# Kernel optimization log

Hardware: AMD Instinct MI355X
Metric: run time of the kernel (lower is better)

The kernel has to match this reference:

```python
import jax, jax.numpy as jnp
import numpy as np

B, T, C, H = 2, 2048, 1024, 16
HD = C // H  # head dim = 64


def setup_inputs() -> dict:
    key = jax.random.key(0)
    k0, k1, k2 = jax.random.split(key, 3)
    x = jax.random.normal(k0, (B, T, C), jnp.float32)
    W_attn = jax.random.normal(k1, (C, 3 * C), jnp.float32) * 0.02
    b_attn = jnp.zeros((3 * C,), jnp.float32)
    W_proj = jax.random.normal(k2, (C, C), jnp.float32) * 0.02
    b_proj = jnp.zeros((C,), jnp.float32)
    # rope: (1,1,T,HD//2,2,2) stack of 2x2 rotation matrices [[cos,-sin],[sin,cos]]
    inv_freq = 1.0 / (10000.0 ** (jnp.arange(0, HD, 2, dtype=jnp.float32) / HD))
    ang = jnp.arange(T, dtype=jnp.float32)[:, None] * inv_freq[None, :]  # (T, HD//2)
    cos, sin = jnp.cos(ang), jnp.sin(ang)
    rope = jnp.stack([jnp.stack([cos, -sin], -1), jnp.stack([sin, cos], -1)], -2)
    rope = rope[None, None]  # (1,1,T,HD//2,2,2)
    return dict(x=x, W_attn=W_attn, b_attn=b_attn, W_proj=W_proj, b_proj=b_proj, rope=rope)


def reference(x, W_attn, b_attn, W_proj, b_proj, rope):
    Bv, Tv, Cv = x.shape
    Hd = Cv // H
    qkv = x @ W_attn + b_attn                      # (B,T,3C) fused QKV proj
    q, k, v = jnp.split(qkv, 3, axis=-1)

    def heads(t):
        return t.reshape(Bv, Tv, H, Hd).transpose(0, 2, 1, 3)  # (B,H,T,Hd)

    q, k, v = heads(q), heads(k), heads(v)

    cos = rope[..., 0, 0][..., None]               # (1,1,T,Hd//2,1)
    sin = rope[..., 1, 0][..., None]

    def rot(t):
        tr = t.reshape(Bv, H, Tv, Hd // 2, 2)
        xr, yr = tr[..., 0:1], tr[..., 1:2]
        out = jnp.concatenate([xr * cos - yr * sin, xr * sin + yr * cos], axis=-1)
        return out.reshape(Bv, H, Tv, Hd)

    q, k = rot(q), rot(k)

    scale = 1.0 / np.sqrt(Hd).astype(np.float32)
    att = jnp.einsum('bhqd,bhkd->bhqk', q, k) * scale
    mask = jnp.tril(jnp.ones((Tv, Tv), dtype=bool))  # causal
    att = jnp.where(mask[None, None], att, -jnp.inf)
    att = jax.nn.softmax(att, axis=-1)
    y = jnp.einsum('bhqk,bhkd->bhqd', att, v)
    y = y.transpose(0, 2, 1, 3).reshape(Bv, Tv, Cv)
    return y @ W_proj + b_proj
```

## Files before the change

kernel.cpp:

```cpp
#include <hip/hip_runtime.h>
#include <hip/hip_bf16.h>

typedef __attribute__((ext_vector_type(8))) short short8;
typedef __attribute__((ext_vector_type(4))) short short4b;
typedef __attribute__((ext_vector_type(4))) float f32x4;
typedef __attribute__((ext_vector_type(16))) float f32x16;
typedef __attribute__((ext_vector_type(4))) unsigned u32x4;

static constexpr int Bb = 2, Tt = 2048, Cc = 1024, Hh = 16;
static constexpr int BT = Bb * Tt;
static constexpr int N1 = 3 * Cc;
static constexpr float QS = 0.125f * 1.44269504f;

__device__ __forceinline__ unsigned short f2b(float f) {
  union { float f; unsigned u; } v; v.f = f;
  unsigned r = v.u + 0x7fffu + ((v.u >> 16) & 1u);
  return (unsigned short)(r >> 16);
}
__device__ __forceinline__ float b2f(short s) {
  union { unsigned u; float f; } v; v.u = ((unsigned)(unsigned short)s) << 16;
  return v.f;
}

__global__ __launch_bounds__(256) void k_cast(const float* __restrict__ in,
                                              unsigned short* __restrict__ out, int n) {
  int i = (blockIdx.x * 256 + threadIdx.x) * 8;
  if (i >= n) return;
  float4 a = *reinterpret_cast<const float4*>(in + i);
  float4 b = *reinterpret_cast<const float4*>(in + i + 4);
  short8 o;
  o[0] = f2b(a.x); o[1] = f2b(a.y); o[2] = f2b(a.z); o[3] = f2b(a.w);
  o[4] = f2b(b.x); o[5] = f2b(b.y); o[6] = f2b(b.z); o[7] = f2b(b.w);
  *reinterpret_cast<short8*>(out + i) = o;
}

__global__ __launch_bounds__(256) void k_tcast(const float* __restrict__ in,
                                               unsigned short* __restrict__ out,
                                               int R, int Ccol) {
  __shared__ float tile[32][33];
  int cb = blockIdx.x * 32, rb = blockIdx.y * 32;
  int tx = threadIdx.x & 31, ty = threadIdx.x >> 5;
  for (int i = 0; i < 32; i += 8)
    tile[ty + i][tx] = in[(size_t)(rb + ty + i) * Ccol + cb + tx];
  __syncthreads();
  for (int i = 0; i < 32; i += 8)
    out[(size_t)(cb + ty + i) * R + rb + tx] = f2b(tile[tx][ty + i]);
}

template <int NF, int EPI>
__global__ __launch_bounds__(512, 2)
void k_gemm8(const unsigned short* __restrict__ A, const unsigned short* __restrict__ Bt,
             const float* __restrict__ bias, void* __restrict__ Cout,
             const float* __restrict__ rope, unsigned short* __restrict__ Qs,
             unsigned short* __restrict__ Ks, unsigned short* __restrict__ Vt,
             int M, int N, int K) {
  constexpr int BN = NF * 64;
  constexpr int ASZ = 256 * 64;
  constexpr int BSZ = BN * 64;
  constexpr int STRIDE = ASZ + BSZ;
  extern __shared__ unsigned short lds[];
  const int tid = threadIdx.x, lane = tid & 63, w = tid >> 6;
  const int wm = w >> 2, wn = w & 3;
  const int l15 = lane & 15, l4 = lane >> 4;
  int nbx = gridDim.x;
  int lin = blockIdx.y * nbx + blockIdx.x;
  int cpx = (nbx * gridDim.y) >> 3;
  lin = (lin & 7) * cpx + (lin >> 3);
  const int mb = lin / nbx, nb = lin % nbx;
  const size_t arow0 = (size_t)mb * 256;
  const size_t brow0 = (size_t)nb * BN;

  const int srow = lane >> 3;
  const int scol = (((lane & 7) * 16) ^ (srow << 4)) >> 1;
  auto stage = [&](int buf, int k0) {
    unsigned short* Ab = lds + buf * STRIDE;
    unsigned short* Bb = Ab + ASZ;
#pragma unroll
    for (int i = 0; i < 4; i++) {
      int c = w + 8 * i;
      const unsigned short* g = A + (arow0 + c * 8 + srow) * (size_t)K + k0 + scol;
      __builtin_amdgcn_global_load_lds((const __attribute__((address_space(1))) void*)g,
          (__attribute__((address_space(3))) void*)(Ab + c * 512), 16, 0, 0);
    }
#pragma unroll
    for (int i = 0; i < NF; i++) {
      int c = w + 8 * i;
      const unsigned short* g = Bt + (brow0 + c * 8 + srow) * (size_t)K + k0 + scol;
      __builtin_amdgcn_global_load_lds((const __attribute__((address_space(1))) void*)g,
          (__attribute__((address_space(3))) void*)(Bb + c * 512), 16, 0, 0);
    }
  };

  f32x4 acc[8][NF] = {};
  const int NK = K >> 6;

  stage(0, 0);
  asm volatile("s_waitcnt vmcnt(0)" ::: "memory");
  asm volatile("s_barrier" ::: "memory");

  for (int kt = 0; kt < NK; kt++) {
    int buf = kt & 1;
    if (kt + 1 < NK) stage(buf ^ 1, (kt + 1) << 6);
    const unsigned short* Ab = lds + buf * STRIDE;
    const unsigned short* Bb = Ab + ASZ;
    short8 af[8][2];
#pragma unroll
    for (int p = 0; p < NF; p++) {
      if (p == 0) {
#pragma unroll
        for (int m = 0; m < 8; m++) {
          int ra = wm * 128 + m * 16 + l15;
#pragma unroll
          for (int kk = 0; kk < 2; kk++) {
            int cb = (kk * 64 + l4 * 16) ^ ((ra & 7) << 4);
            af[m][kk] = *reinterpret_cast<const short8*>(Ab + ra * 64 + (cb >> 1));
          }
        }
      }
      short8 bfr[2];
      int rb = wn * (NF * 16) + p * 16 + l15;
#pragma unroll
      for (int kk = 0; kk < 2; kk++) {
        int cb = (kk * 64 + l4 * 16) ^ ((rb & 7) << 4);
        bfr[kk] = *reinterpret_cast<const short8*>(Bb + rb * 64 + (cb >> 1));
      }
      asm volatile("s_barrier" ::: "memory");
      asm volatile("s_waitcnt lgkmcnt(0)" ::: "memory");
      __builtin_amdgcn_sched_barrier(0);
      __builtin_amdgcn_s_setprio(1);
#pragma unroll
      for (int m = 0; m < 8; m++) {
        acc[m][p] = __builtin_amdgcn_mfma_f32_16x16x32_bf16(af[m][0], bfr[0], acc[m][p], 0, 0, 0);
        acc[m][p] = __builtin_amdgcn_mfma_f32_16x16x32_bf16(af[m][1], bfr[1], acc[m][p], 0, 0, 0);
      }
      __builtin_amdgcn_s_setprio(0);
      if (p == NF - 1)
        asm volatile("s_waitcnt vmcnt(0)" ::: "memory");
      asm volatile("s_barrier" ::: "memory");
    }
  }

#pragma unroll
  for (int m = 0; m < 8; m++) {
#pragma unroll
    for (int n = 0; n < NF; n++) {
      int ccol0 = nb * BN + wn * (NF * 16) + n * 16;
      float bv = bias[ccol0 + l15];
      int r0 = mb * 256 + wm * 128 + m * 16 + l4 * 4;
      if (EPI == 0) {
#pragma unroll
        for (int j = 0; j < 4; j++)
          ((float*)Cout)[(size_t)(r0 + j) * N + ccol0 + l15] = acc[m][n][j] + bv;
      } else {
        int cls = ccol0 >> 10;
        int h = (ccol0 >> 6) & 15;
        int d = (ccol0 & 63) + l15;
        int bq = r0 >> 11;
        int t0 = r0 & 2047;
        size_t bh = (size_t)bq * 16 + h;
        if (cls == 2) {
          short4b o;
#pragma unroll
          for (int j = 0; j < 4; j++) o[j] = (short)f2b(acc[m][n][j] + bv);
          *reinterpret_cast<short4b*>(Vt + (bh * 64 + d) * Tt + t0) = o;
        } else {
          unsigned short* dst = (cls == 0) ? Qs : Ks;
          int jj = d >> 1;
          int odd = d & 1;
#pragma unroll
          for (int j = 0; j < 4; j++) {
            float v = acc[m][n][j] + bv;
            float part = __shfl_xor(v, 1);
            float2 sc = *reinterpret_cast<const float2*>(
                rope + (size_t)(t0 + j) * 128 + jj * 4 + 2);
            float x = odd ? part : v;
            float y = odd ? v : part;
            float rot = odd ? (x * sc.x + y * sc.y)
                            : (x * sc.y - y * sc.x);
            if (cls == 0) rot *= QS;
            dst[(bh * Tt + (t0 + j)) * 64 + d] = f2b(rot);
          }
        }
      }
    }
  }
}

__device__ __forceinline__ float tmax16(const f32x16& v) {
  float a0 = fmaxf(v[0], v[1]),   a1 = fmaxf(v[2], v[3]);
  float a2 = fmaxf(v[4], v[5]),   a3 = fmaxf(v[6], v[7]);
  float a4 = fmaxf(v[8], v[9]),   a5 = fmaxf(v[10], v[11]);
  float a6 = fmaxf(v[12], v[13]), a7 = fmaxf(v[14], v[15]);
  float b0 = fmaxf(a0, a1), b1 = fmaxf(a2, a3), b2 = fmaxf(a4, a5), b3 = fmaxf(a6, a7);
  return fmaxf(fmaxf(b0, b1), fmaxf(b2, b3));
}

__device__ __forceinline__ void attn_tile64(
    const unsigned short* Kl, const unsigned short* Vl,
    int w, int l31, int hi, const short8 qf[4],
    float& m_run, float& l_run, f32x16 oacc[2], int grelBase) {
  f32x16 sc[2];
  bool act[2];
#pragma unroll
  for (int kt = 0; kt < 2; kt++) {
    int grel = grelBase + kt;
    act[kt] = (grel <= w);
    if (!act[kt]) continue;
    f32x16 acc = {};
    int rk = kt * 32 + l31;
    int sw = (rk & 7) << 4;
    const unsigned short* krow = Kl + rk * 64;
    short8 kf[4];
#pragma unroll
    for (int kk = 0; kk < 4; kk++)
      kf[kk] = *reinterpret_cast<const short8*>(krow + (((kk * 32 + hi * 16) ^ sw) >> 1));
    __builtin_amdgcn_s_setprio(1);
#pragma unroll
    for (int kk = 0; kk < 4; kk++)
      acc = __builtin_amdgcn_mfma_f32_32x32x16_bf16(kf[kk], qf[kk], acc, 0, 0, 0);
    __builtin_amdgcn_s_setprio(0);
    if (grel == w) {
#pragma unroll
      for (int r = 0; r < 16; r++) {
        int e = (r & 3) + 8 * (r >> 2) + 4 * hi;
        if (e > l31) acc[r] = -1e30f;
      }
    }
    sc[kt] = acc;
  }
  float km0 = act[0] ? tmax16(sc[0]) : -1e30f;
  float km1 = act[1] ? tmax16(sc[1]) : -1e30f;
  float mx = fmaxf(km0, km1);
  mx = fmaxf(mx, __shfl_xor(mx, 32));

  float fsc = 1.f;
  if (!__all(mx <= m_run + 8.f)) {
    float nm = fmaxf(m_run, mx);
    fsc = __builtin_amdgcn_exp2f(m_run - nm);
    m_run = nm;
#pragma unroll
    for (int dt = 0; dt < 2; dt++)
#pragma unroll
      for (int r = 0; r < 16; r++) oacc[dt][r] *= fsc;
  }

  float kps[2] = {0.f, 0.f};
#pragma unroll
  for (int kt = 0; kt < 2; kt++) {
    if (!act[kt]) continue;
    float p[16];
#pragma unroll
    for (int r = 0; r < 16; r++) p[r] = __builtin_amdgcn_exp2f(sc[kt][r] - m_run);
    float s0 = (p[0] + p[1]) + (p[2] + p[3]);
    float s1 = (p[4] + p[5]) + (p[6] + p[7]);
    float s2 = (p[8] + p[9]) + (p[10] + p[11]);
    float s3 = (p[12] + p[13]) + (p[14] + p[15]);
    kps[kt] = (s0 + s1) + (s2 + s3);
    unsigned P[8];
#pragma unroll
    for (int i = 0; i < 8; i++)
      asm("v_cvt_pk_bf16_f32 %0, %1, %2" : "=v"(P[i]) : "v"(p[2 * i]), "v"(p[2 * i + 1]));
    unsigned Y0 = (unsigned)__shfl_xor((int)(hi ? P[0] : P[2]), 32);
    unsigned Y1 = (unsigned)__shfl_xor((int)(hi ? P[1] : P[3]), 32);
    unsigned Y2 = (unsigned)__shfl_xor((int)(hi ? P[4] : P[6]), 32);
    unsigned Y3 = (unsigned)__shfl_xor((int)(hi ? P[5] : P[7]), 32);
    u32x4 c0 = hi ? u32x4{Y0, Y1, P[2], P[3]} : u32x4{P[0], P[1], Y0, Y1};
    u32x4 c1 = hi ? u32x4{Y2, Y3, P[6], P[7]} : u32x4{P[4], P[5], Y2, Y3};
    short8 pf0 = __builtin_bit_cast(short8, c0);
    short8 pf1 = __builtin_bit_cast(short8, c1);
#pragma unroll
    for (int dt = 0; dt < 2; dt++) {
      int d = dt * 32 + l31;
      int sv = (d & 7) << 4;
      const unsigned short* vrow = Vl + d * 64;
      short8 vf0 = *reinterpret_cast<const short8*>(vrow + (((kt * 64 + hi * 16) ^ sv) >> 1));
      short8 vf1 = *reinterpret_cast<const short8*>(vrow + (((kt * 64 + 32 + hi * 16) ^ sv) >> 1));
      __builtin_amdgcn_s_setprio(1);
      oacc[dt] = __builtin_amdgcn_mfma_f32_32x32x16_bf16(vf0, pf0, oacc[dt], 0, 0, 0);
      oacc[dt] = __builtin_amdgcn_mfma_f32_32x32x16_bf16(vf1, pf1, oacc[dt], 0, 0, 0);
      __builtin_amdgcn_s_setprio(0);
    }
  }
  float psum = kps[0] + kps[1];
  psum += __shfl_xor(psum, 32);
  l_run = l_run * fsc + psum;
}

__global__ __launch_bounds__(256)
void k_attn1(const unsigned short* __restrict__ Qs, const unsigned short* __restrict__ Ks,
             const unsigned short* __restrict__ Vt, unsigned short* __restrict__ Opart,
             float* __restrict__ ml) {
  __shared__ unsigned short lds[16384];
  int tid = threadIdx.x, lane = tid & 63, w = tid >> 6;
  int sid = blockIdx.x;
  int qb = 15 - (sid >> 6);
  int c = (sid >> 5) & 1;
  int bh = sid & 31;
  int l31 = lane & 31, hi = lane >> 5;
  int qw0 = qb * 128 + w * 32;
  const unsigned short* Qb = Qs + (size_t)bh * Tt * 64;
  const unsigned short* Kb = Ks + (size_t)bh * Tt * 64;
  const unsigned short* Vb = Vt + (size_t)bh * 64 * Tt;

  const int NT = 2 * qb + 2;
  const int half = NT >> 1;
  const int t0 = c ? half : 0;
  const int t1 = c ? NT : half;

  auto stage = [&](int buf, int kv0) {
    unsigned short* Kbuf = lds + buf * 4096;
    unsigned short* Vbuf = lds + 8192 + buf * 4096;
    int r8 = lane >> 3;
    int colb = ((lane & 7) * 16) ^ (r8 << 4);
#pragma unroll
    for (int cc = 0; cc < 2; cc++) {
      int ch = w + cc * 4;
      const unsigned short* gk = Kb + (size_t)(kv0 + ch * 8 + r8) * 64 + (colb >> 1);
      __builtin_amdgcn_global_load_lds((const __attribute__((address_space(1))) void*)gk,
          (__attribute__((address_space(3))) void*)(Kbuf + ch * 512), 16, 0, 0);
      const unsigned short* gv = Vb + (size_t)(ch * 8 + r8) * Tt + kv0 + (colb >> 1);
      __builtin_amdgcn_global_load_lds((const __attribute__((address_space(1))) void*)gv,
          (__attribute__((address_space(3))) void*)(Vbuf + ch * 512), 16, 0, 0);
    }
  };

  short8 qf[4];
#pragma unroll
  for (int kk = 0; kk < 4; kk++)
    qf[kk] = *reinterpret_cast<const short8*>(Qb + (size_t)(qw0 + l31) * 64 + kk * 16 + hi * 8);

  float m_run = -1e30f, l_run = 0.f;
  f32x16 oacc[2] = {};

  stage(0, t0 * 64);
  __syncthreads();
  int cur = 0;
  for (int T = t0; T < t1; ++T) {
    if (T + 1 < t1) stage(cur ^ 1, (T + 1) * 64);
    attn_tile64(lds + cur * 4096, lds + 8192 + cur * 4096,
                w, l31, hi, qf, m_run, l_run, oacc, 2 * T - 4 * qb);
    __syncthreads();
    cur ^= 1;
  }

  size_t orow = (size_t)sid * 128 + w * 32 + l31;
#pragma unroll
  for (int dt = 0; dt < 2; dt++)
#pragma unroll
    for (int q4 = 0; q4 < 4; q4++) {
      short4b oo;
#pragma unroll
      for (int jj = 0; jj < 4; jj++) oo[jj] = (short)f2b(oacc[dt][q4 * 4 + jj]);
      *reinterpret_cast<short4b*>(Opart + orow * 64 + dt * 32 + q4 * 8 + hi * 4) = oo;
    }
  if (hi == 0) {
    float2 v; v.x = m_run; v.y = l_run;
    *reinterpret_cast<float2*>(ml + orow * 2) = v;
  }
}

__global__ __launch_bounds__(256)
void k_attn2(const unsigned short* __restrict__ Opart, const float* __restrict__ ml,
             unsigned short* __restrict__ Y) {
  int gid = blockIdx.x * 256 + threadIdx.x;
  int row = gid >> 3;
  int dblk = (gid & 7) * 8;
  int bh = row >> 11, q = row & 2047;
  int qb = q >> 7, qrow = q & 127;
  int s0 = (15 - qb) * 64 + bh;
  int s1 = s0 + 32;
  float2 ml0 = *reinterpret_cast<const float2*>(ml + ((size_t)s0 * 128 + qrow) * 2);
  float2 ml1 = *reinterpret_cast<const float2*>(ml + ((size_t)s1 * 128 + qrow) * 2);
  float m = fmaxf(ml0.x, ml1.x);
  float w0 = __builtin_amdgcn_exp2f(ml0.x - m);
  float w1 = __builtin_amdgcn_exp2f(ml1.x - m);
  float inv = 1.0f / (w0 * ml0.y + w1 * ml1.y);
  float a0 = w0 * inv, a1 = w1 * inv;
  short8 o0 = *reinterpret_cast<const short8*>(Opart + ((size_t)s0 * 128 + qrow) * 64 + dblk);
  short8 o1 = *reinterpret_cast<const short8*>(Opart + ((size_t)s1 * 128 + qrow) * 64 + dblk);
  short8 o;
#pragma unroll
  for (int j = 0; j < 8; j++) o[j] = (short)f2b(b2f(o0[j]) * a0 + b2f(o1[j]) * a1);
  int b = bh >> 4, h = bh & 15;
  *reinterpret_cast<short8*>(Y + ((size_t)(b * Tt + q)) * Cc + h * 64 + dblk) = o;
}

extern "C" void kernel_launch(void* const* d_in, const int* in_sizes, int n_in,
                              void* d_out, int out_size, void* d_ws, size_t ws_size,
                              hipStream_t stream) {
  (void)in_sizes; (void)n_in; (void)out_size; (void)ws_size;
  const float* x      = (const float*)d_in[0];
  const float* W_attn = (const float*)d_in[1];
  const float* b_attn = (const float*)d_in[2];
  const float* W_proj = (const float*)d_in[3];
  const float* b_proj = (const float*)d_in[4];
  const float* rope   = (const float*)d_in[5];
  float* out = (float*)d_out;

  char* ws = (char*)d_ws;
  unsigned short* xb    = (unsigned short*)(ws);
  unsigned short* WaT   = (unsigned short*)(ws + (8u << 20));
  unsigned short* WpT   = (unsigned short*)(ws + (14u << 20));
  unsigned short* Qs    = (unsigned short*)(ws + (16u << 20));
  unsigned short* Ks    = (unsigned short*)(ws + (24u << 20));
  unsigned short* Vt    = (unsigned short*)(ws + (32u << 20));
  unsigned short* Yb    = (unsigned short*)(ws + (40u << 20));
  unsigned short* Opart = (unsigned short*)(ws + (48u << 20));
  float*          ml    = (float*)(ws + (64u << 20));

  constexpr int LDS_QKV  = (256 + 192) * 64 * 2 * 2;
  constexpr int LDS_PROJ = (256 + 128) * 64 * 2 * 2;
  (void)hipFuncSetAttribute(reinterpret_cast<const void*>(&k_gemm8<3, 1>),
                            hipFuncAttributeMaxDynamicSharedMemorySize, LDS_QKV);
  (void)hipFuncSetAttribute(reinterpret_cast<const void*>(&k_gemm8<2, 0>),
                            hipFuncAttributeMaxDynamicSharedMemorySize, LDS_PROJ);

  k_cast<<<2048, 256, 0, stream>>>(x, xb, BT * Cc);
  k_tcast<<<dim3(N1 / 32, Cc / 32), 256, 0, stream>>>(W_attn, WaT, Cc, N1);
  k_tcast<<<dim3(Cc / 32, Cc / 32), 256, 0, stream>>>(W_proj, WpT, Cc, Cc);
  k_gemm8<3, 1><<<dim3(N1 / 192, BT / 256), 512, LDS_QKV, stream>>>(
      xb, WaT, b_attn, nullptr, rope, Qs, Ks, Vt, BT, N1, Cc);
  k_attn1<<<1024, 256, 0, stream>>>(Qs, Ks, Vt, Opart, ml);
  k_attn2<<<2048, 256, 0, stream>>>(Opart, ml, Yb);
  k_gemm8<2, 0><<<dim3(Cc / 128, BT / 256), 512, LDS_PROJ, stream>>>(
      Yb, WpT, b_proj, out, nullptr, nullptr, nullptr, nullptr, BT, Cc, Cc);
}
```

Before: 118.2 us.

## Replace double-buffered GEMM with a four-slot LDS ring pipeline and retile

The QKV and output-projection GEMMs move from a double-buffered kernel with 64-wide K steps to a templated kernel. It keeps a four-slot LDS ring of 32-wide K steps, three stages in flight, and one barrier per step. The aim is to hide global-load latency better and to cut the per-fragment barriers of the old loop. Tile shapes also change: QKV now uses 256x256 tiles, which gives fewer blocks than the CU count, and projection uses 128x128 tiles with 4 waves. The larger LDS footprint and fewer QKV blocks may reduce occupancy and parallelism.

```diff
diff --git a/kernel.cpp b/kernel.cpp
--- a/kernel.cpp
+++ b/kernel.cpp
@@ -47,110 +47,99 @@
     out[(size_t)(cb + ty + i) * R + rb + tx] = f2b(tile[tx][ty + i]);
 }
 
-template <int NF, int EPI>
-__global__ __launch_bounds__(512, 2)
-void k_gemm8(const unsigned short* __restrict__ A, const unsigned short* __restrict__ Bt,
-             const float* __restrict__ bias, void* __restrict__ Cout,
-             const float* __restrict__ rope, unsigned short* __restrict__ Qs,
-             unsigned short* __restrict__ Ks, unsigned short* __restrict__ Vt,
-             int M, int N, int K) {
-  constexpr int BN = NF * 64;
-  constexpr int ASZ = 256 * 64;
-  constexpr int BSZ = BN * 64;
-  constexpr int STRIDE = ASZ + BSZ;
-  extern __shared__ unsigned short lds[];
+template <int BM, int BN, int WM, int WN, int EPI>
+__global__ __launch_bounds__(WM * WN * 64, 2)
+void k_ring(const unsigned short* __restrict__ A, const unsigned short* __restrict__ Bt,
+            const float* __restrict__ bias, float* __restrict__ Cout,
+            const float* __restrict__ rope, unsigned short* __restrict__ Qs,
+            unsigned short* __restrict__ Ks, unsigned short* __restrict__ Vt,
+            int N, int K) {
+  constexpr int NW = WM * WN;
+  constexpr int MF = BM / WM / 16;
+  constexpr int NF = BN / WN / 16;
+  constexpr int ASZ = BM * 32;
+  constexpr int SLOT = ASZ + BN * 32;
+  extern __shared__ unsigned short ring[];
   const int tid = threadIdx.x, lane = tid & 63, w = tid >> 6;
-  const int wm = w >> 2, wn = w & 3;
+  const int wm = w / WN, wn = w % WN;
   const int l15 = lane & 15, l4 = lane >> 4;
-  int nbx = gridDim.x;
+  const int nbx = gridDim.x;
   int lin = blockIdx.y * nbx + blockIdx.x;
   int cpx = (nbx * gridDim.y) >> 3;
   lin = (lin & 7) * cpx + (lin >> 3);
   const int mb = lin / nbx, nb = lin % nbx;
-  const size_t arow0 = (size_t)mb * 256;
-  const size_t brow0 = (size_t)nb * BN;
-
-  const int srow = lane >> 3;
-  const int scol = (((lane & 7) * 16) ^ (srow << 4)) >> 1;
-  auto stage = [&](int buf, int k0) {
-    unsigned short* Ab = lds + buf * STRIDE;
-    unsigned short* Bb = Ab + ASZ;
-#pragma unroll
-    for (int i = 0; i < 4; i++) {
-      int c = w + 8 * i;
-      const unsigned short* g = A + (arow0 + c * 8 + srow) * (size_t)K + k0 + scol;
-      __builtin_amdgcn_global_load_lds((const __attribute__((address_space(1))) void*)g,
-          (__attribute__((address_space(3))) void*)(Ab + c * 512), 16, 0, 0);
-    }
-#pragma unroll
-    for (int i = 0; i < NF; i++) {
-      int c = w + 8 * i;
-      const unsigned short* g = Bt + (brow0 + c * 8 + srow) * (size_t)K + k0 + scol;
-      __builtin_amdgcn_global_load_lds((const __attribute__((address_space(1))) void*)g,
-          (__attribute__((address_space(3))) void*)(Bb + c * 512), 16, 0, 0);
+  const size_t arow0 = (size_t)mb * BM, brow0 = (size_t)nb * BN;
+
+  const int rsub = lane >> 2;
+  const int gcol8 = ((lane & 3) ^ (rsub & 3)) * 8;
+  auto stage = [&](int v) {
+    unsigned short* s = ring + (v & 3) * SLOT;
+#pragma unroll
+    for (int i = 0; i < 2; i++) {
+      int c = w + i * NW;
+      int row = c * 16 + rsub;
+      const unsigned short* gA = A + (arow0 + row) * (size_t)K + v * 32 + gcol8;
+      __builtin_amdgcn_global_load_lds((const __attribute__((address_space(1))) void*)gA,
+          (__attribute__((address_space(3))) void*)(s + c * 512), 16, 0, 0);
+      const unsigned short* gB = Bt + (brow0 + row) * (size_t)K + v * 32 + gcol8;
+      __builtin_amdgcn_global_load_lds((const __attribute__((address_space(1))) void*)gB,
+          (__attribute__((address_space(3))) void*)(s + ASZ + c * 512), 16, 0, 0);
     }
   };
 
-  f32x4 acc[8][NF] = {};
-  const int NK = K >> 6;
-
-  stage(0, 0);
+  f32x4 acc[MF][NF] = {};
+  const int fcol8 = (l4 ^ (l15 & 3)) * 8;
+
+  auto compute = [&](int u) {
+    const unsigned short* As = ring + (u & 3) * SLOT;
+    const unsigned short* Bs = As + ASZ;
+    short8 af[MF], bf[NF];
+#pragma unroll
+    for (int m = 0; m < MF; m++)
+      af[m] = *reinterpret_cast<const short8*>(As + (wm * (BM / WM) + m * 16 + l15) * 32 + fcol8);
+#pragma unroll
+    for (int n = 0; n < NF; n++)
+      bf[n] = *reinterpret_cast<const short8*>(Bs + (wn * (BN / WN) + n * 16 + l15) * 32 + fcol8);
+    asm volatile("s_waitcnt lgkmcnt(0)" ::: "memory");
+    __builtin_amdgcn_sched_barrier(0);
+    __builtin_amdgcn_s_setprio(1);
+#pragma unroll
+    for (int m = 0; m < MF; m++)
+#pragma unroll
+      for (int n = 0; n < NF; n++)
+        acc[m][n] = __builtin_amdgcn_mfma_f32_16x16x32_bf16(af[m], bf[n], acc[m][n], 0, 0, 0);
+    __builtin_amdgcn_s_setprio(0);
+  };
+
+  const int KU = K >> 5;
+  stage(0); stage(1); stage(2);
+  asm volatile("s_waitcnt vmcnt(8)" ::: "memory");
+  asm volatile("s_barrier" ::: "memory");
+  for (int u = 0; u < KU - 3; ++u) {
+    stage(u + 3);
+    compute(u);
+    asm volatile("s_waitcnt vmcnt(8)" ::: "memory");
+    asm volatile("s_barrier" ::: "memory");
+  }
+  compute(KU - 3);
+  asm volatile("s_waitcnt vmcnt(4)" ::: "memory");
+  asm volatile("s_barrier" ::: "memory");
+  compute(KU - 2);
   asm volatile("s_waitcnt vmcnt(0)" ::: "memory");
   asm volatile("s_barrier" ::: "memory");
-
-  for (int kt = 0; kt < NK; kt++) {
-    int buf = kt & 1;
-    if (kt + 1 < NK) stage(buf ^ 1, (kt + 1) << 6);
-    const unsigned short* Ab = lds + buf * STRIDE;
-    const unsigned short* Bb = Ab + ASZ;
-    short8 af[8][2];
-#pragma unroll
-    for (int p = 0; p < NF; p++) {
-      if (p == 0) {
-#pragma unroll
-        for (int m = 0; m < 8; m++) {
-          int ra = wm * 128 + m * 16 + l15;
-#pragma unroll
-          for (int kk = 0; kk < 2; kk++) {
-            int cb = (kk * 64 + l4 * 16) ^ ((ra & 7) << 4);
-            af[m][kk] = *reinterpret_cast<const short8*>(Ab + ra * 64 + (cb >> 1));
-          }
-        }
-      }
-      short8 bfr[2];
-      int rb = wn * (NF * 16) + p * 16 + l15;
-#pragma unroll
-      for (int kk = 0; kk < 2; kk++) {
-        int cb = (kk * 64 + l4 * 16) ^ ((rb & 7) << 4);
-        bfr[kk] = *reinterpret_cast<const short8*>(Bb + rb * 64 + (cb >> 1));
-      }
-      asm volatile("s_barrier" ::: "memory");
-      asm volatile("s_waitcnt lgkmcnt(0)" ::: "memory");
-      __builtin_amdgcn_sched_barrier(0);
-      __builtin_amdgcn_s_setprio(1);
-#pragma unroll
-      for (int m = 0; m < 8; m++) {
-        acc[m][p] = __builtin_amdgcn_mfma_f32_16x16x32_bf16(af[m][0], bfr[0], acc[m][p], 0, 0, 0);
-        acc[m][p] = __builtin_amdgcn_mfma_f32_16x16x32_bf16(af[m][1], bfr[1], acc[m][p], 0, 0, 0);
-      }
-      __builtin_amdgcn_s_setprio(0);
-      if (p == NF - 1)
-        asm volatile("s_waitcnt vmcnt(0)" ::: "memory");
-      asm volatile("s_barrier" ::: "memory");
-    }
-  }
-
-#pragma unroll
-  for (int m = 0; m < 8; m++) {
+  compute(KU - 1);
+
+#pragma unroll
+  for (int m = 0; m < MF; m++) {
 #pragma unroll
     for (int n = 0; n < NF; n++) {
-      int ccol0 = nb * BN + wn * (NF * 16) + n * 16;
+      int ccol0 = nb * BN + wn * (BN / WN) + n * 16;
       float bv = bias[ccol0 + l15];
-      int r0 = mb * 256 + wm * 128 + m * 16 + l4 * 4;
+      int r0 = mb * BM + wm * (BM / WM) + m * 16 + l4 * 4;
       if (EPI == 0) {
 #pragma unroll
         for (int j = 0; j < 4; j++)
-          ((float*)Cout)[(size_t)(r0 + j) * N + ccol0 + l15] = acc[m][n][j] + bv;
+          Cout[(size_t)(r0 + j) * N + ccol0 + l15] = acc[m][n][j] + bv;
       } else {
         int cls = ccol0 >> 10;
         int h = (ccol0 >> 6) & 15;
@@ -408,20 +397,20 @@
   unsigned short* Opart = (unsigned short*)(ws + (48u << 20));
   float*          ml    = (float*)(ws + (64u << 20));
 
-  constexpr int LDS_QKV  = (256 + 192) * 64 * 2 * 2;
-  constexpr int LDS_PROJ = (256 + 128) * 64 * 2 * 2;
-  (void)hipFuncSetAttribute(reinterpret_cast<const void*>(&k_gemm8<3, 1>),
+  constexpr int LDS_QKV  = 4 * (256 + 256) * 32 * 2;
+  constexpr int LDS_PROJ = 4 * (128 + 128) * 32 * 2;
+  (void)hipFuncSetAttribute(reinterpret_cast<const void*>(&k_ring<256, 256, 2, 4, 1>),
                             hipFuncAttributeMaxDynamicSharedMemorySize, LDS_QKV);
-  (void)hipFuncSetAttribute(reinterpret_cast<const void*>(&k_gemm8<2, 0>),
+  (void)hipFuncSetAttribute(reinterpret_cast<const void*>(&k_ring<128, 128, 2, 2, 0>),
                             hipFuncAttributeMaxDynamicSharedMemorySize, LDS_PROJ);
 
   k_cast<<<2048, 256, 0, stream>>>(x, xb, BT * Cc);
   k_tcast<<<dim3(N1 / 32, Cc / 32), 256, 0, stream>>>(W_attn, WaT, Cc, N1);
   k_tcast<<<dim3(Cc / 32, Cc / 32), 256, 0, stream>>>(W_proj, WpT, Cc, Cc);
-  k_gemm8<3, 1><<<dim3(N1 / 192, BT / 256), 512, LDS_QKV, stream>>>(
-      xb, WaT, b_attn, nullptr, rope, Qs, Ks, Vt, BT, N1, Cc);
+  k_ring<256, 256, 2, 4, 1><<<dim3(N1 / 256, BT / 256), 512, LDS_QKV, stream>>>(
+      xb, WaT, b_attn, nullptr, rope, Qs, Ks, Vt, N1, Cc);
   k_attn1<<<1024, 256, 0, stream>>>(Qs, Ks, Vt, Opart, ml);
   k_attn2<<<2048, 256, 0, stream>>>(Opart, ml, Yb);
-  k_gemm8<2, 0><<<dim3(Cc / 128, BT / 256), 512, LDS_PROJ, stream>>>(
-      Yb, WpT, b_proj, out, nullptr, nullptr, nullptr, nullptr, BT, Cc, Cc);
-}
+  k_ring<128, 128, 2, 2, 0><<<dim3(Cc / 128, BT / 128), 256, LDS_PROJ, stream>>>(
+      Yb, WpT, b_proj, out, nullptr, nullptr, nullptr, nullptr, Cc, Cc);
+}
```

New measurement: 121.5 us. 2.8% more time.
